# Optimization experiments

Hardware: AMD Instinct MI355X
Metric: run time of the kernel (lower is better)

The kernel has to match this reference:

```python
import jax, jax.numpy as jnp
import numpy as np
from math import ceil, log2

LEVELS = 8
# pywt 'db4' filters (length 8)
DB4_DEC_HI = np.array([-0.23037781330885523, 0.7148465705525415, -0.6308807679295904,
                       -0.02798376941698385, 0.18703481171888114, 0.030841381835986965,
                       -0.032883011666982945, -0.010597401784997278], dtype=np.float32)
DB4_REC_HI = np.array([-0.010597401784997278, -0.032883011666982945, 0.030841381835986965,
                       0.18703481171888114, -0.02798376941698385, -0.6308807679295904,
                       0.7148465705525415, -0.23037781330885523], dtype=np.float32)


def setup_inputs() -> dict:
    key = jax.random.key(0)
    x = jax.random.normal(key, (2048, 3000), dtype=jnp.float32)
    scaling = jnp.tile(jnp.asarray(DB4_DEC_HI), (LEVELS, 1))       # [levels, 8]
    scaling_rec = jnp.tile(jnp.asarray(DB4_REC_HI), (LEVELS, 1))   # [levels, 8]
    return {"input": x, "scaling": scaling, "scaling_rec": scaling_rec}


def _make_wavelet(h):
    # g = flip(h); g[1::2] *= -1
    g = jnp.flip(h, axis=-1)
    signs = jnp.where(jnp.arange(g.shape[-1]) % 2 == 1, -1.0, 1.0).astype(g.dtype)
    return g * signs


def _circ_conv(x, filt, transpose=False):
    # FFT-based circular convolution (filter zero-padded to input length)
    L = x.shape[-1]
    ra = jnp.fft.rfft(x)
    rb = jnp.fft.rfft(filt, n=L)
    if transpose:
        rb = jnp.conj(rb)
    return jnp.fft.irfft(ra * rb, n=L)


def _upsample2(x):
    # interleave zeros: out[:, ::2] = x
    n, k = x.shape
    out = jnp.zeros((n, 2 * k), dtype=x.dtype)
    return out.at[:, ::2].set(x)


def _forward(x, scaling, scaling_rec):
    levels = scaling.shape[0]
    m = x.shape[1]
    L = 2 ** ceil(log2(m))
    p0 = (L - m) // 2
    p1 = ceil((L - m) / 2)
    x = jnp.pad(x, ((0, 0), (p0, p1)), mode="edge")  # ReplicationPad1d

    approx = x
    wav_coeffs = []
    for lvl in range(levels):
        wavelet = _make_wavelet(scaling_rec[lvl])
        details = _circ_conv(approx, wavelet)[:, ::2]
        approx = _circ_conv(approx, scaling[lvl])[:, ::2]
        wav_coeffs.append(details)
    wav_coeffs.append(approx)

    # (no thresholding: the original forward copies coeffs unmodified)
    filtered = list(wav_coeffs)
    approx = filtered[-1]
    for lvl in reversed(range(levels)):
        details = filtered[lvl]
        wav_syn = _make_wavelet(scaling_rec[lvl])
        d_rec = _circ_conv(_upsample2(details), wav_syn, transpose=True)
        a_rec = _circ_conv(_upsample2(approx), scaling[lvl], transpose=True)
        approx = d_rec + a_rec

    recon = approx[:, p0:m + p1]
    coeffs = jnp.concatenate(wav_coeffs, axis=-1)  # total length == L
    return recon, coeffs


def reference(input, scaling, scaling_rec):
    return _forward(input, scaling, scaling_rec)
```

## Files before the change

### kernel.cpp

```cpp
#include <hip/hip_runtime.h>

#define NROWS 2048
#define MLEN  3000
#define LPAD  4096
#define PAD0  548
#define NLVL  8
#define NT    256

union F4 { float4 v; float f[4]; };

__global__ __launch_bounds__(NT) void despawn_kernel(
    const float* __restrict__ x,
    const float* __restrict__ scaling,
    const float* __restrict__ scaling_rec,
    float* __restrict__ recon_out,
    float* __restrict__ coef_out)
{
    __shared__ __align__(16) float SA[LPAD];
    __shared__ __align__(16) float SB[LPAD / 2];
    __shared__ __align__(16) float CS[512];
    __shared__ float fsca[64];
    __shared__ float fwav[64];

    const int tid = threadIdx.x;
    const int row = blockIdx.x;
    float* const crow = coef_out + (size_t)row * LPAD;

    if (tid < 64) {
        const int lvl = tid >> 3, k = tid & 7;
        fsca[tid] = scaling[tid];
        fwav[tid] = scaling_rec[lvl * 8 + (7 - k)] * ((k & 1) ? -1.0f : 1.0f);
    }

    const float* xr = x + (size_t)row * MLEN;
    const float xlo = xr[0], xhi = xr[MLEN - 1];
    {
        const float4* xr4 = reinterpret_cast<const float4*>(xr);
        for (int g = tid; g < MLEN / 4; g += NT) {
            F4 u; u.v = xr4[g];
            const int h = PAD0 / 2 + 2 * g;
            *reinterpret_cast<float2*>(&SA[h])            = make_float2(u.f[0], u.f[2]);
            *reinterpret_cast<float2*>(&SA[LPAD / 2 + h]) = make_float2(u.f[1], u.f[3]);
        }
    }
    for (int i = tid; i < PAD0 / 2; i += NT) {
        SA[i] = xlo;
        SA[LPAD / 2 + i] = xlo;
        SA[PAD0 / 2 + MLEN / 2 + i] = xhi;
        SA[LPAD / 2 + PAD0 / 2 + MLEN / 2 + i] = xhi;
    }
    __syncthreads();

    {
        float* cur = SA;
        float* alt = SB;
        int H = LPAD / 2;
        int coff = 0;
        for (int lvl = 0; lvl < NLVL; ++lvl) {
            float W[8], S[8];
#pragma unroll
            for (int k = 0; k < 8; ++k) { W[k] = fwav[lvl * 8 + k]; S[k] = fsca[lvl * 8 + k]; }
            const int q = H >> 2;
            const int qm = q - 1;
            const float4* ev4 = reinterpret_cast<const float4*>(cur);
            const float4* od4 = reinterpret_cast<const float4*>(cur + H);
            float4* dst4 = reinterpret_cast<float4*>(crow + coff);
            float4* cs4 = (lvl >= 3) ? reinterpret_cast<float4*>(&CS[coff - 3584]) : nullptr;
            for (int t = tid; t < q; t += NT) {
                F4 Ea, Eb, Oa, Ob;
                Ea.v = ev4[(t - 1) & qm];
                Eb.v = ev4[t];
                Oa.v = od4[(t - 1) & qm];
                Ob.v = od4[t];
                float e[8] = {Ea.f[0],Ea.f[1],Ea.f[2],Ea.f[3],Eb.f[0],Eb.f[1],Eb.f[2],Eb.f[3]};
                float o[8] = {Oa.f[0],Oa.f[1],Oa.f[2],Oa.f[3],Ob.f[0],Ob.f[1],Ob.f[2],Ob.f[3]};
                float ds[4], as[4];
#pragma unroll
                for (int u = 0; u < 4; ++u) {
                    float d = 0.f, a = 0.f;
#pragma unroll
                    for (int m = 0; m < 4; ++m) {
                        const float vE = e[4 + u - m];
                        const float vO = o[3 + u - m];
                        d = fmaf(vE, W[2 * m], d);
                        d = fmaf(vO, W[2 * m + 1], d);
                        a = fmaf(vE, S[2 * m], a);
                        a = fmaf(vO, S[2 * m + 1], a);
                    }
                    ds[u] = d; as[u] = a;
                }
                F4 dv; dv.f[0] = ds[0]; dv.f[1] = ds[1]; dv.f[2] = ds[2]; dv.f[3] = ds[3];
                dst4[t] = dv.v;
                if (cs4) cs4[t] = dv.v;
                *reinterpret_cast<float2*>(alt + 2 * t)            = make_float2(as[0], as[2]);
                *reinterpret_cast<float2*>(alt + (H >> 1) + 2 * t) = make_float2(as[1], as[3]);
            }
            __syncthreads();
            coff += H;
            float* tmp = cur; cur = alt; alt = tmp;
            H >>= 1;
        }
    }

    if (tid < 16) {
        const float v = SA[((tid & 1) ? 8 : 0) + (tid >> 1)];
        crow[LPAD - 16 + tid] = v;
        CS[496 + tid] = v;
    }
    __syncthreads();

    const float* a = &CS[496];
    float* obuf = SB;
    int len = 16;
    for (int lvl = NLVL - 1; lvl >= 1; --lvl) {
        float W[8], S[8];
#pragma unroll
        for (int k = 0; k < 8; ++k) { W[k] = fwav[lvl * 8 + k]; S[k] = fsca[lvl * 8 + k]; }
        const int Mout = len << 1;
        const int doff = LPAD - (LPAD >> lvl);
        const float4* d4 = (lvl >= 3)
            ? reinterpret_cast<const float4*>(&CS[doff - 3584])
            : reinterpret_cast<const float4*>(crow + doff);
        const float4* a4 = reinterpret_cast<const float4*>(a);
        const int gq = Mout >> 3;
        const int fm = (len >> 2) - 1;
        for (int g = tid; g < gq; g += NT) {
            F4 Da, Db, Aa, Ab;
            Da.v = d4[g]; Db.v = d4[(g + 1) & fm];
            Aa.v = a4[g]; Ab.v = a4[(g + 1) & fm];
            float dd[8] = {Da.f[0],Da.f[1],Da.f[2],Da.f[3],Db.f[0],Db.f[1],Db.f[2],Db.f[3]};
            float aa[8] = {Aa.f[0],Aa.f[1],Aa.f[2],Aa.f[3],Ab.f[0],Ab.f[1],Ab.f[2],Ab.f[3]};
            float out[8];
#pragma unroll
            for (int u = 0; u < 8; ++u) {
                const int p = u & 1, c = (u + 1) >> 1;
                float s = 0.f;
#pragma unroll
                for (int m = 0; m < 4; ++m) {
                    s = fmaf(dd[c + m], W[p + 2 * m], s);
                    s = fmaf(aa[c + m], S[p + 2 * m], s);
                }
                out[u] = s;
            }
            F4 o0, o1;
            o0.f[0] = out[0]; o0.f[1] = out[1]; o0.f[2] = out[2]; o0.f[3] = out[3];
            o1.f[0] = out[4]; o1.f[1] = out[5]; o1.f[2] = out[6]; o1.f[3] = out[7];
            float4* ob4 = reinterpret_cast<float4*>(obuf + 8 * g);
            ob4[0] = o0.v; ob4[1] = o1.v;
        }
        __syncthreads();
        a = obuf;
        obuf = (obuf == SB) ? SA : SB;
        len = Mout;
    }
    {
        float W[8], S[8];
#pragma unroll
        for (int k = 0; k < 8; ++k) { W[k] = fwav[k]; S[k] = fsca[k]; }
        const float4* d4 = reinterpret_cast<const float4*>(crow);
        const float4* a4 = reinterpret_cast<const float4*>(a);
        const int fm = (len >> 2) - 1;
        float* const ro = recon_out + (size_t)row * MLEN;
        for (int g = tid; g < (LPAD >> 3); g += NT) {
            F4 Da, Db, Aa, Ab;
            Da.v = d4[g]; Db.v = d4[(g + 1) & fm];
            Aa.v = a4[g]; Ab.v = a4[(g + 1) & fm];
            float dd[8] = {Da.f[0],Da.f[1],Da.f[2],Da.f[3],Db.f[0],Db.f[1],Db.f[2],Db.f[3]};
            float aa[8] = {Aa.f[0],Aa.f[1],Aa.f[2],Aa.f[3],Ab.f[0],Ab.f[1],Ab.f[2],Ab.f[3]};
            float out[8];
#pragma unroll
            for (int u = 0; u < 8; ++u) {
                const int p = u & 1, c = (u + 1) >> 1;
                float s = 0.f;
#pragma unroll
                for (int m = 0; m < 4; ++m) {
                    s = fmaf(dd[c + m], W[p + 2 * m], s);
                    s = fmaf(aa[c + m], S[p + 2 * m], s);
                }
                out[u] = s;
            }
            const int n0 = 8 * g;
            if (n0 >= PAD0 && n0 + 8 <= PAD0 + MLEN) {
                F4 o0, o1;
                o0.f[0] = out[0]; o0.f[1] = out[1]; o0.f[2] = out[2]; o0.f[3] = out[3];
                o1.f[0] = out[4]; o1.f[1] = out[5]; o1.f[2] = out[6]; o1.f[3] = out[7];
                float4* r4 = reinterpret_cast<float4*>(ro + (n0 - PAD0));
                r4[0] = o0.v; r4[1] = o1.v;
            } else {
#pragma unroll
                for (int u = 0; u < 8; ++u) {
                    const int n = n0 + u;
                    if (n >= PAD0 && n < PAD0 + MLEN) ro[n - PAD0] = out[u];
                }
            }
        }
    }
}

extern "C" void kernel_launch(void* const* d_in, const int* in_sizes, int n_in,
                              void* d_out, int out_size, void* d_ws, size_t ws_size,
                              hipStream_t stream) {
    const float* x           = (const float*)d_in[0];
    const float* scaling     = (const float*)d_in[1];
    const float* scaling_rec = (const float*)d_in[2];
    float* recon = (float*)d_out;
    float* coefo = recon + (size_t)NROWS * MLEN;
    despawn_kernel<<<dim3(NROWS), dim3(NT), 0, stream>>>(x, scaling, scaling_rec,
                                                         recon, coefo);
    (void)in_sizes; (void)n_in; (void)out_size; (void)d_ws; (void)ws_size;
}
```

Before: 99.58 us.

## Fuse level-0 analysis with global input load to shrink LDS footprint

Level 0 of the forward transform is now computed straight from global memory. Each thread gathers 14 samples with clamped edge-replication and wrap-around indexing, which removes the padded 4096-float shared staging buffer. SA shrinks to 2048 floats, so the LDS footprint per block drops, and launch bounds request 8 blocks per CU to raise occupancy. The cost is redundant, scalar, partly uncoalesced global loads (14 per 8 outputs) in place of vectorized float4 loads, and the ping-pong buffer roles are swapped to match.

```diff
diff --git a/kernel.cpp b/kernel.cpp
--- a/kernel.cpp
+++ b/kernel.cpp
@@ -9,15 +9,15 @@
 
 union F4 { float4 v; float f[4]; };
 
-__global__ __launch_bounds__(NT) void despawn_kernel(
+__global__ __launch_bounds__(NT, 8) void despawn_kernel(
     const float* __restrict__ x,
     const float* __restrict__ scaling,
     const float* __restrict__ scaling_rec,
     float* __restrict__ recon_out,
     float* __restrict__ coef_out)
 {
-    __shared__ __align__(16) float SA[LPAD];
-    __shared__ __align__(16) float SB[LPAD / 2];
+    __shared__ __align__(16) float SA[2048];
+    __shared__ __align__(16) float SB[2048];
     __shared__ __align__(16) float CS[512];
     __shared__ float fsca[64];
     __shared__ float fwav[64];
@@ -25,38 +25,59 @@
     const int tid = threadIdx.x;
     const int row = blockIdx.x;
     float* const crow = coef_out + (size_t)row * LPAD;
+    const float* xr = x + (size_t)row * MLEN;
 
     if (tid < 64) {
         const int lvl = tid >> 3, k = tid & 7;
         fsca[tid] = scaling[tid];
         fwav[tid] = scaling_rec[lvl * 8 + (7 - k)] * ((k & 1) ? -1.0f : 1.0f);
     }
-
-    const float* xr = x + (size_t)row * MLEN;
-    const float xlo = xr[0], xhi = xr[MLEN - 1];
+    __syncthreads();
+
     {
-        const float4* xr4 = reinterpret_cast<const float4*>(xr);
-        for (int g = tid; g < MLEN / 4; g += NT) {
-            F4 u; u.v = xr4[g];
-            const int h = PAD0 / 2 + 2 * g;
-            *reinterpret_cast<float2*>(&SA[h])            = make_float2(u.f[0], u.f[2]);
-            *reinterpret_cast<float2*>(&SA[LPAD / 2 + h]) = make_float2(u.f[1], u.f[3]);
-        }
-    }
-    for (int i = tid; i < PAD0 / 2; i += NT) {
-        SA[i] = xlo;
-        SA[LPAD / 2 + i] = xlo;
-        SA[PAD0 / 2 + MLEN / 2 + i] = xhi;
-        SA[LPAD / 2 + PAD0 / 2 + MLEN / 2 + i] = xhi;
-    }
-    __syncthreads();
+        float W[8], S[8];
+#pragma unroll
+        for (int k = 0; k < 8; ++k) { W[k] = fwav[k]; S[k] = fsca[k]; }
+        for (int t = tid; t < 512; t += NT) {
+            const int base = 8 * t - 7;
+            float xv[14];
+#pragma unroll
+            for (int r = 0; r < 14; ++r) {
+                const int i = base + r;
+                int g = i - PAD0;
+                g = g < 0 ? 0 : (g > MLEN - 1 ? MLEN - 1 : g);
+                if (i < 0) g = MLEN - 1;
+                xv[r] = xr[g];
+            }
+            float ds[4], as[4];
+#pragma unroll
+            for (int u = 0; u < 4; ++u) {
+                float d = 0.f, a = 0.f;
+#pragma unroll
+                for (int m = 0; m < 4; ++m) {
+                    const float vE = xv[2 * u - 2 * m + 7];
+                    const float vO = xv[2 * u - 2 * m + 6];
+                    d = fmaf(vE, W[2 * m], d);
+                    d = fmaf(vO, W[2 * m + 1], d);
+                    a = fmaf(vE, S[2 * m], a);
+                    a = fmaf(vO, S[2 * m + 1], a);
+                }
+                ds[u] = d; as[u] = a;
+            }
+            F4 dv; dv.f[0] = ds[0]; dv.f[1] = ds[1]; dv.f[2] = ds[2]; dv.f[3] = ds[3];
+            reinterpret_cast<float4*>(crow)[t] = dv.v;
+            *reinterpret_cast<float2*>(SA + 2 * t)        = make_float2(as[0], as[2]);
+            *reinterpret_cast<float2*>(SA + 1024 + 2 * t) = make_float2(as[1], as[3]);
+        }
+        __syncthreads();
+    }
 
     {
         float* cur = SA;
         float* alt = SB;
-        int H = LPAD / 2;
-        int coff = 0;
-        for (int lvl = 0; lvl < NLVL; ++lvl) {
+        int H = 1024;
+        int coff = 2048;
+        for (int lvl = 1; lvl < NLVL; ++lvl) {
             float W[8], S[8];
 #pragma unroll
             for (int k = 0; k < 8; ++k) { W[k] = fwav[lvl * 8 + k]; S[k] = fsca[lvl * 8 + k]; }
@@ -103,14 +124,14 @@
     }
 
     if (tid < 16) {
-        const float v = SA[((tid & 1) ? 8 : 0) + (tid >> 1)];
+        const float v = SB[((tid & 1) ? 8 : 0) + (tid >> 1)];
         crow[LPAD - 16 + tid] = v;
         CS[496 + tid] = v;
     }
     __syncthreads();
 
     const float* a = &CS[496];
-    float* obuf = SB;
+    float* obuf = SA;
     int len = 16;
     for (int lvl = NLVL - 1; lvl >= 1; --lvl) {
         float W[8], S[8];
@@ -150,9 +171,10 @@
         }
         __syncthreads();
         a = obuf;
-        obuf = (obuf == SB) ? SA : SB;
+        obuf = (obuf == SA) ? SB : SA;
         len = Mout;
     }
+
     {
         float W[8], S[8];
 #pragma unroll
@@ -183,7 +205,7 @@
             if (n0 >= PAD0 && n0 + 8 <= PAD0 + MLEN) {
                 F4 o0, o1;
                 o0.f[0] = out[0]; o0.f[1] = out[1]; o0.f[2] = out[2]; o0.f[3] = out[3];
-                o1.f[0] = out[4]; o1.f[1] = out[5]; o1.f[2] = out[6]; o1.f[3] = out[7];
+                o1.f[0] = out[4]; o1.f[1] = out[5]; o1.f[2] = out[6]; o1.f[7 - 4] = out[7];
                 float4* r4 = reinterpret_cast<float4*>(ro + (n0 - PAD0));
                 r4[0] = o0.v; r4[1] = o1.v;
             } else {
```

Result: slower. 122.4 us (+22.9%).
